# Performance work log

Hardware: AMD Instinct MI355X
Metric: run time of the kernel (lower is better)

The kernel has to match this reference:

```python
import jax, jax.numpy as jnp
import numpy as np

N = 50000
E = 800000
H = 4
C = 64
EPS = 1e-5

def _gat_layer(x, W, a_src, a_dst, bias, src, dst, n):
    # x: [N, F_in]; W: [F_in, H*C]
    h = (x @ W).reshape(n, H, C)                      # [N,H,C]
    asrc = jnp.einsum('nhc,hc->nh', h, a_src)         # [N,H]
    adst = jnp.einsum('nhc,hc->nh', h, a_dst)         # [N,H]
    e = jax.nn.leaky_relu(asrc[src] + adst[dst], 0.2) # [E,H]
    emax = jax.ops.segment_max(e, dst, num_segments=n)
    e = jnp.exp(e - emax[dst])
    denom = jax.ops.segment_sum(e, dst, num_segments=n)
    alpha = e / (denom[dst] + 1e-16)                  # [E,H]
    msg = h[src] * alpha[:, :, None]                  # [E,H,C]
    out = jax.ops.segment_sum(msg, dst, num_segments=n)
    return out.reshape(n, H * C) + bias

def _bn_eval(x, gamma, beta, mean, var):
    return (x - mean) * jax.lax.rsqrt(var + EPS) * gamma + beta

def setup_inputs() -> dict:
    key = jax.random.key(0)
    ks = jax.random.split(key, 12)
    d = {}
    d['x'] = jax.random.normal(ks[0], (N, 128), jnp.float32)
    d['edge_index'] = jax.random.randint(ks[1], (2, E), 0, N, jnp.int32)
    d['W1'] = jax.random.normal(ks[2], (128, H * C), jnp.float32) * 0.05
    d['a_src1'] = jax.random.normal(ks[3], (H, C), jnp.float32) * 0.05
    d['a_dst1'] = jax.random.normal(ks[4], (H, C), jnp.float32) * 0.05
    d['b1'] = jnp.zeros((H * C,), jnp.float32)
    d['g1'] = jax.random.uniform(ks[5], (H * C,), jnp.float32, 0.5, 1.5)
    d['be1'] = jnp.zeros((H * C,), jnp.float32)
    d['m1'] = jnp.zeros((H * C,), jnp.float32)
    d['v1'] = jax.random.uniform(ks[6], (H * C,), jnp.float32, 0.5, 1.5)
    d['W2'] = jax.random.normal(ks[7], (H * C, H * C), jnp.float32) * 0.05
    d['a_src2'] = jax.random.normal(ks[8], (H, C), jnp.float32) * 0.05
    d['a_dst2'] = jax.random.normal(ks[9], (H, C), jnp.float32) * 0.05
    d['b2'] = jnp.zeros((H * C,), jnp.float32)
    d['g2'] = jax.random.uniform(ks[10], (H * C,), jnp.float32, 0.5, 1.5)
    d['be2'] = jnp.zeros((H * C,), jnp.float32)
    d['m2'] = jnp.zeros((H * C,), jnp.float32)
    d['v2'] = jax.random.uniform(ks[11], (H * C,), jnp.float32, 0.5, 1.5)
    return d

def reference(x, edge_index, W1, a_src1, a_dst1, b1, g1, be1, m1, v1,
              W2, a_src2, a_dst2, b2, g2, be2, m2, v2):
    # PyG GATConv default: add self-loops
    loops = jnp.arange(N, dtype=edge_index.dtype)
    src = jnp.concatenate([edge_index[0], loops])
    dst = jnp.concatenate([edge_index[1], loops])
    h = _gat_layer(x, W1, a_src1, a_dst1, b1, src, dst, N)
    h = jax.nn.relu(_bn_eval(h, g1, be1, m1, v1))  # dropout identity at eval
    h = _gat_layer(h, W2, a_src2, a_dst2, b2, src, dst, N)
    h = jax.nn.relu(_bn_eval(h, g2, be2, m2, v2))
    return jax.nn.log_softmax(h, axis=1)
```

## Files before the change

kernel.cpp:

```cpp
#include <hip/hip_runtime.h>
#include <hip/hip_bf16.h>
#include <cstdint>

#define N_NODES 50000
#define N_EDGES 800000
#define ET_EDGES (N_EDGES + N_NODES)
#define FDIM 256
#define BN_EPS 1e-5f
#define CAP 96

typedef short bf16x8 __attribute__((ext_vector_type(8)));
typedef float f32x4 __attribute__((ext_vector_type(4)));

__device__ __forceinline__ float lrelu(float x) { return x >= 0.f ? x : 0.2f * x; }
__device__ __forceinline__ float b2f(unsigned short u) {
    return __uint_as_float(((unsigned int)u) << 16);
}
__device__ __forceinline__ unsigned short f2b(float f) {
    unsigned int u = __float_as_uint(f);
    u += 0x7fffu + ((u >> 16) & 1u);
    return (unsigned short)(u >> 16);
}

__device__ __forceinline__ void acc_i8(float acc8[8], int2 p, float c) {
#pragma unroll
    for (int k = 0; k < 4; ++k)
        acc8[k] = fmaf((float)((signed char)(p.x >> (8 * k))), c, acc8[k]);
#pragma unroll
    for (int k = 0; k < 4; ++k)
        acc8[k + 4] = fmaf((float)((signed char)(p.y >> (8 * k))), c, acc8[k + 4]);
}

#define NB_CONV 6250
#define NB_WT1  128
#define NB_WT2  256
#define NB_DEGZ 196
__global__ __launch_bounds__(256) void setup_kernel(
        const float* __restrict__ x, unsigned short* __restrict__ xb,
        const float* __restrict__ W1, unsigned short* __restrict__ W1T,
        const float* __restrict__ W2, unsigned short* __restrict__ W2T,
        int* __restrict__ cursor,
        const float* __restrict__ b1, const float* __restrict__ g1,
        const float* __restrict__ be1, const float* __restrict__ m1,
        const float* __restrict__ v1,
        const float* __restrict__ b2, const float* __restrict__ g2,
        const float* __restrict__ be2, const float* __restrict__ m2,
        const float* __restrict__ v2,
        float* sc1, float* sh1, float* sc2, float* sh2) {
    int b = blockIdx.x, tid = threadIdx.x;
    if (b < NB_CONV) {
        int i = b * 256 + tid;
        float4 v = ((const float4*)x)[i];
        ushort4 o;
        o.x = f2b(v.x); o.y = f2b(v.y); o.z = f2b(v.z); o.w = f2b(v.w);
        ((ushort4*)xb)[i] = o;
    } else if (b < NB_CONV + NB_WT1) {
        int t = (b - NB_CONV) * 256 + tid;
        int n = t >> 7, k = t & 127;
        W1T[t] = f2b(W1[(size_t)k * 256 + n]);
    } else if (b < NB_CONV + NB_WT1 + NB_WT2) {
        int t = (b - NB_CONV - NB_WT1) * 256 + tid;
        int n = t >> 8, k = t & 255;
        W2T[t] = f2b(W2[(size_t)k * 256 + n]);
    } else if (b < NB_CONV + NB_WT1 + NB_WT2 + NB_DEGZ) {
        int i = (b - NB_CONV - NB_WT1 - NB_WT2) * 256 + tid;
        if (i < N_NODES) cursor[i] = 0;
    } else {
        int f = tid;
        float s1 = rsqrtf(v1[f] + BN_EPS) * g1[f];
        sc1[f] = s1;
        sh1[f] = (b1[f] - m1[f]) * s1 + be1[f];
        float s2 = rsqrtf(v2[f] + BN_EPS) * g2[f];
        sc2[f] = s2;
        sh2[f] = (b2[f] - m2[f]) * s2 + be2[f];
    }
}

__global__ __launch_bounds__(256) void scatter_kernel(const int* __restrict__ ei,
                                                      int* __restrict__ cursor,
                                                      int* __restrict__ csr) {
    int e = blockIdx.x * 256 + threadIdx.x;
    if (e >= ET_EDGES) return;
    int s, d;
    if (e < N_EDGES) { s = ei[e]; d = ei[N_EDGES + e]; }
    else             { s = d = e - N_EDGES; }
    int pos = atomicAdd(&cursor[d], 1);
    if (pos < CAP) csr[d * CAP + pos] = s;
}

template <int K>
__global__ __launch_bounds__(512) void gemm_fused_kernel(
        const unsigned short* __restrict__ A,
        const unsigned short* __restrict__ BT,
        const float* __restrict__ a_src, const float* __restrict__ a_dst,
        signed char* __restrict__ H8, float* __restrict__ scaleRow,
        float* __restrict__ asrc, float* __restrict__ adst, int M) {
    constexpr int BK = 64;
    __shared__ unsigned short As[128][BK + 8];
    __shared__ unsigned short Bs[256][BK + 8];
    __shared__ int amaxL[128];
    const int tid = threadIdx.x;
    const int lane = tid & 63;
    const int w = tid >> 6;
    const int bm = blockIdx.x * 128;
    const int wr = (w >> 2) * 64;
    const int wc = (w & 3) * 64;
    const int hd = w & 3;
    if (tid < 128) amaxL[tid] = 0;

    f32x4 acc[4][4];
#pragma unroll
    for (int i = 0; i < 4; ++i)
#pragma unroll
        for (int j = 0; j < 4; ++j) acc[i][j] = (f32x4){0.f, 0.f, 0.f, 0.f};

    const int srow = tid >> 3;
    const int skc = (tid & 7) * 8;

    for (int k0 = 0; k0 < K; k0 += BK) {
#pragma unroll
        for (int i = 0; i < 2; ++i) {
            int row = i * 64 + srow;
            int ar = bm + row; if (ar >= M) ar = M - 1;
            *(bf16x8*)&As[row][skc] = *(const bf16x8*)(A + (size_t)ar * K + k0 + skc);
        }
#pragma unroll
        for (int i = 0; i < 4; ++i) {
            int row = i * 64 + srow;
            *(bf16x8*)&Bs[row][skc] = *(const bf16x8*)(BT + (size_t)row * K + k0 + skc);
        }
        __syncthreads();
#pragma unroll
        for (int ks = 0; ks < BK; ks += 32) {
            const int kk = ks + (lane >> 4) * 8;
            bf16x8 af[4], bfr[4];
#pragma unroll
            for (int i = 0; i < 4; ++i) {
                af[i]  = *(const bf16x8*)&As[wr + i * 16 + (lane & 15)][kk];
                bfr[i] = *(const bf16x8*)&Bs[wc + i * 16 + (lane & 15)][kk];
            }
#pragma unroll
            for (int i = 0; i < 4; ++i)
#pragma unroll
                for (int j = 0; j < 4; ++j)
                    acc[i][j] = __builtin_amdgcn_mfma_f32_16x16x32_bf16(af[i], bfr[j], acc[i][j], 0, 0, 0);
        }
        __syncthreads();
    }

    const int q = lane >> 4, c16 = lane & 15;
#pragma unroll
    for (int i = 0; i < 4; ++i) {
#pragma unroll
        for (int r = 0; r < 4; ++r) {
            float a = fmaxf(fmaxf(fabsf(acc[i][0][r]), fabsf(acc[i][1][r])),
                            fmaxf(fabsf(acc[i][2][r]), fabsf(acc[i][3][r])));
#pragma unroll
            for (int off = 1; off < 16; off <<= 1) a = fmaxf(a, __shfl_xor(a, off));
            if (c16 == 0) atomicMax(&amaxL[wr + i * 16 + q * 4 + r], __float_as_int(a));
        }
    }
    __syncthreads();

    float asv[4], adv[4];
#pragma unroll
    for (int j = 0; j < 4; ++j) {
        int c = j * 16 + c16;
        asv[j] = a_src[hd * 64 + c];
        adv[j] = a_dst[hd * 64 + c];
    }
#pragma unroll
    for (int i = 0; i < 4; ++i) {
#pragma unroll
        for (int r = 0; r < 4; ++r) {
            int lrow = wr + i * 16 + q * 4 + r;
            int gr = bm + lrow;
            float amax = __int_as_float(amaxL[lrow]);
            float rcpS = amax > 1e-20f ? 127.f / amax : 0.f;
            if (gr < M) {
#pragma unroll
                for (int j = 0; j < 4; ++j) {
                    int qv = (int)rintf(acc[i][j][r] * rcpS);
                    H8[(size_t)gr * 256 + wc + j * 16 + c16] = (signed char)qv;
                }
                if (c16 == 0 && (w & 3) == 0) scaleRow[gr] = amax * (1.f / 127.f);
            }
            float p_s = acc[i][0][r] * asv[0] + acc[i][1][r] * asv[1]
                      + acc[i][2][r] * asv[2] + acc[i][3][r] * asv[3];
            float p_d = acc[i][0][r] * adv[0] + acc[i][1][r] * adv[1]
                      + acc[i][2][r] * adv[2] + acc[i][3][r] * adv[3];
#pragma unroll
            for (int off = 1; off < 16; off <<= 1) {
                p_s += __shfl_xor(p_s, off);
                p_d += __shfl_xor(p_d, off);
            }
            if (c16 == 0 && gr < M) {
                asrc[(size_t)gr * 4 + hd] = p_s;
                adst[(size_t)gr * 4 + hd] = p_d;
            }
        }
    }
}

template <bool FINAL>
__device__ __forceinline__ void gat_epilogue(const float acc8[8], int fl, bool doStore,
                                             int node, const float* __restrict__ scale,
                                             const float* __restrict__ shift,
                                             float* __restrict__ outf,
                                             unsigned short* __restrict__ outb) {
    float4 scA = ((const float4*)scale)[fl * 2], scB = ((const float4*)scale)[fl * 2 + 1];
    float4 shA = ((const float4*)shift)[fl * 2], shB = ((const float4*)shift)[fl * 2 + 1];
    float t[8];
    t[0] = fmaxf(fmaf(acc8[0], scA.x, shA.x), 0.f);
    t[1] = fmaxf(fmaf(acc8[1], scA.y, shA.y), 0.f);
    t[2] = fmaxf(fmaf(acc8[2], scA.z, shA.z), 0.f);
    t[3] = fmaxf(fmaf(acc8[3], scA.w, shA.w), 0.f);
    t[4] = fmaxf(fmaf(acc8[4], scB.x, shB.x), 0.f);
    t[5] = fmaxf(fmaf(acc8[5], scB.y, shB.y), 0.f);
    t[6] = fmaxf(fmaf(acc8[6], scB.z, shB.z), 0.f);
    t[7] = fmaxf(fmaf(acc8[7], scB.w, shB.w), 0.f);
    if (FINAL) {
        float m = t[0];
#pragma unroll
        for (int k = 1; k < 8; ++k) m = fmaxf(m, t[k]);
#pragma unroll
        for (int off = 1; off < 32; off <<= 1) m = fmaxf(m, __shfl_xor(m, off));
        float es = 0.f;
#pragma unroll
        for (int k = 0; k < 8; ++k) es += __expf(t[k] - m);
#pragma unroll
        for (int off = 1; off < 32; off <<= 1) es += __shfl_xor(es, off);
        float lse = m + logf(es);
        if (doStore) {
            float* p = outf + (size_t)node * 256 + fl * 8;
            *(float4*)p = make_float4(t[0] - lse, t[1] - lse, t[2] - lse, t[3] - lse);
            *(float4*)(p + 4) = make_float4(t[4] - lse, t[5] - lse, t[6] - lse, t[7] - lse);
        }
    } else {
        if (doStore) {
            bf16x8 ob;
#pragma unroll
            for (int k = 0; k < 8; ++k) ob[k] = (short)f2b(t[k]);
            *(bf16x8*)(outb + (size_t)node * 256 + fl * 8) = ob;
        }
    }
}

template <bool FINAL>
__global__ __launch_bounds__(256) void gat_gather_kernel(const int* __restrict__ cursor,
                                                         const int* __restrict__ csr,
                                                         const float* __restrict__ asrc,
                                                         const float* __restrict__ adst,
                                                         const float* __restrict__ scaleRow,
                                                         const signed char* __restrict__ h8,
                                                         const float* __restrict__ scale,
                                                         const float* __restrict__ shift,
                                                         float* __restrict__ outf,
                                                         unsigned short* __restrict__ outb) {
    __shared__ int src_l[4][64];
    __shared__ float al[4][4][65];

    const int wid = threadIdx.x >> 6;
    const int lane = threadIdx.x & 63;
    const int nodeBase = blockIdx.x * 8 + wid * 2;
    if (nodeBase >= N_NODES) return;
    const int g = lane >> 5, l32 = lane & 31;

    {
        int node = nodeBase + g;
        bool valid = node < N_NODES;
        int nodeC = valid ? node : N_NODES - 1;
        int deg = valid ? min(cursor[nodeC], CAP) : 0;
        int beg = nodeC * CAP;
        int dmax = max(deg, __shfl_xor(deg, 32));

        if (dmax <= 32) {
            float4 ad = *(const float4*)(adst + (size_t)nodeC * 4);
            int s = 0;
            float sc = 0.f;
            float c0 = -3.4e38f, c1 = -3.4e38f, c2 = -3.4e38f, c3 = -3.4e38f;
            if (l32 < deg) {
                s = csr[beg + l32];
                sc = scaleRow[s];
                float4 as = *(const float4*)(asrc + (size_t)s * 4);
                c0 = lrelu(as.x + ad.x); c1 = lrelu(as.y + ad.y);
                c2 = lrelu(as.z + ad.z); c3 = lrelu(as.w + ad.w);
            }
            float m0 = c0, m1 = c1, m2 = c2, m3 = c3;
#pragma unroll
            for (int off = 1; off < 32; off <<= 1) {
                m0 = fmaxf(m0, __shfl_xor(m0, off)); m1 = fmaxf(m1, __shfl_xor(m1, off));
                m2 = fmaxf(m2, __shfl_xor(m2, off)); m3 = fmaxf(m3, __shfl_xor(m3, off));
            }
            float e0 = 0.f, e1 = 0.f, e2 = 0.f, e3 = 0.f;
            if (l32 < deg) {
                e0 = __expf(c0 - m0); e1 = __expf(c1 - m1);
                e2 = __expf(c2 - m2); e3 = __expf(c3 - m3);
            }
            float s0 = e0, s1 = e1, s2 = e2, s3 = e3;
#pragma unroll
            for (int off = 1; off < 32; off <<= 1) {
                s0 += __shfl_xor(s0, off); s1 += __shfl_xor(s1, off);
                s2 += __shfl_xor(s2, off); s3 += __shfl_xor(s3, off);
            }
            src_l[wid][lane] = s;
            al[wid][0][lane] = e0 / (s0 + 1e-16f) * sc;
            al[wid][1][lane] = e1 / (s1 + 1e-16f) * sc;
            al[wid][2][lane] = e2 / (s2 + 1e-16f) * sc;
            al[wid][3][lane] = e3 / (s3 + 1e-16f) * sc;
            __asm__ volatile("s_waitcnt lgkmcnt(0)" ::: "memory");

            const int base = g * 32;
            const int hsel = l32 >> 3;
            float acc8[8];
#pragma unroll
            for (int k = 0; k < 8; ++k) acc8[k] = 0.f;

            int e = 0;
            for (; e + 7 < deg; e += 8) {
                int sv[8]; float av[8]; int2 hv[8];
#pragma unroll
                for (int u = 0; u < 8; ++u) {
                    sv[u] = src_l[wid][base + e + u];
                    av[u] = al[wid][hsel][base + e + u];
                }
#pragma unroll
                for (int u = 0; u < 8; ++u)
                    hv[u] = *(const int2*)(h8 + (size_t)sv[u] * 256 + l32 * 8);
#pragma unroll
                for (int u = 0; u < 8; ++u) acc_i8(acc8, hv[u], av[u]);
            }
            for (; e + 3 < deg; e += 4) {
                int sv[4]; float av[4]; int2 hv[4];
#pragma unroll
                for (int u = 0; u < 4; ++u) {
                    sv[u] = src_l[wid][base + e + u];
                    av[u] = al[wid][hsel][base + e + u];
                }
#pragma unroll
                for (int u = 0; u < 4; ++u)
                    hv[u] = *(const int2*)(h8 + (size_t)sv[u] * 256 + l32 * 8);
#pragma unroll
                for (int u = 0; u < 4; ++u) acc_i8(acc8, hv[u], av[u]);
            }
            for (; e < deg; ++e) {
                int sA = src_l[wid][base + e];
                float aA = al[wid][hsel][base + e];
                int2 hA = *(const int2*)(h8 + (size_t)sA * 256 + l32 * 8);
                acc_i8(acc8, hA, aA);
            }
            gat_epilogue<FINAL>(acc8, l32, valid, node, scale, shift, outf, outb);
            return;
        }
    }

    const int half = lane >> 5;
    const int fl = lane & 31;
    const int hsel = fl >> 3;
    for (int t = 0; t < 2; ++t) {
        int node = nodeBase + t;
        if (node >= N_NODES) break;
        int deg = min(cursor[node], CAP);
        int beg = node * CAP, end = beg + deg;
        float4 ad = *(const float4*)(adst + (size_t)node * 4);
        float acc8[8];
#pragma unroll
        for (int k = 0; k < 8; ++k) acc8[k] = 0.f;

        if (deg <= 64) {
            int s = 0;
            float sc = 0.f;
            float c0 = -3.4e38f, c1 = -3.4e38f, c2 = -3.4e38f, c3 = -3.4e38f;
            if (lane < deg) {
                s = csr[beg + lane];
                sc = scaleRow[s];
                float4 as = *(const float4*)(asrc + (size_t)s * 4);
                c0 = lrelu(as.x + ad.x); c1 = lrelu(as.y + ad.y);
                c2 = lrelu(as.z + ad.z); c3 = lrelu(as.w + ad.w);
            }
            float m0 = c0, m1 = c1, m2 = c2, m3 = c3;
#pragma unroll
            for (int off = 1; off < 64; off <<= 1) {
                m0 = fmaxf(m0, __shfl_xor(m0, off)); m1 = fmaxf(m1, __shfl_xor(m1, off));
                m2 = fmaxf(m2, __shfl_xor(m2, off)); m3 = fmaxf(m3, __shfl_xor(m3, off));
            }
            float e0 = 0.f, e1 = 0.f, e2 = 0.f, e3 = 0.f;
            if (lane < deg) {
                e0 = __expf(c0 - m0); e1 = __expf(c1 - m1);
                e2 = __expf(c2 - m2); e3 = __expf(c3 - m3);
            }
            float s0 = e0, s1 = e1, s2 = e2, s3 = e3;
#pragma unroll
            for (int off = 1; off < 64; off <<= 1) {
                s0 += __shfl_xor(s0, off); s1 += __shfl_xor(s1, off);
                s2 += __shfl_xor(s2, off); s3 += __shfl_xor(s3, off);
            }
            src_l[wid][lane] = s;
            al[wid][0][lane] = e0 / (s0 + 1e-16f) * sc;
            al[wid][1][lane] = e1 / (s1 + 1e-16f) * sc;
            al[wid][2][lane] = e2 / (s2 + 1e-16f) * sc;
            al[wid][3][lane] = e3 / (s3 + 1e-16f) * sc;
            __asm__ volatile("s_waitcnt lgkmcnt(0)" ::: "memory");

            int e = 0;
            for (; e + 1 < deg; e += 2) {
                int iA = e + half;
                int sA = src_l[wid][iA];
                float aA = al[wid][hsel][iA];
                int2 hA = *(const int2*)(h8 + (size_t)sA * 256 + fl * 8);
                acc_i8(acc8, hA, aA);
            }
            if (e < deg) {
                int idx = e + half;
                int sA = src_l[wid][0];
                float aA = 0.f;
                if (idx < deg) { sA = src_l[wid][idx]; aA = al[wid][hsel][idx]; }
                int2 hA = *(const int2*)(h8 + (size_t)sA * 256 + fl * 8);
                acc_i8(acc8, hA, aA);
            }
#pragma unroll
            for (int k = 0; k < 8; ++k) acc8[k] += __shfl_xor(acc8[k], 32);
        } else {
            float m0 = -3.4e38f, m1 = -3.4e38f, m2 = -3.4e38f, m3 = -3.4e38f;
            for (int e = beg + lane; e < end; e += 64) {
                int s = csr[e];
                float4 as = *(const float4*)(asrc + (size_t)s * 4);
                m0 = fmaxf(m0, lrelu(as.x + ad.x)); m1 = fmaxf(m1, lrelu(as.y + ad.y));
                m2 = fmaxf(m2, lrelu(as.z + ad.z)); m3 = fmaxf(m3, lrelu(as.w + ad.w));
            }
#pragma unroll
            for (int off = 1; off < 64; off <<= 1) {
                m0 = fmaxf(m0, __shfl_xor(m0, off)); m1 = fmaxf(m1, __shfl_xor(m1, off));
                m2 = fmaxf(m2, __shfl_xor(m2, off)); m3 = fmaxf(m3, __shfl_xor(m3, off));
            }
            float s0 = 0.f, s1 = 0.f, s2 = 0.f, s3 = 0.f;
            for (int e = beg + lane; e < end; e += 64) {
                int s = csr[e];
                float4 as = *(const float4*)(asrc + (size_t)s * 4);
                s0 += __expf(lrelu(as.x + ad.x) - m0); s1 += __expf(lrelu(as.y + ad.y) - m1);
                s2 += __expf(lrelu(as.z + ad.z) - m2); s3 += __expf(lrelu(as.w + ad.w) - m3);
            }
#pragma unroll
            for (int off = 1; off < 64; off <<= 1) {
                s0 += __shfl_xor(s0, off); s1 += __shfl_xor(s1, off);
                s2 += __shfl_xor(s2, off); s3 += __shfl_xor(s3, off);
            }
            float mh = (hsel == 0) ? m0 : (hsel == 1) ? m1 : (hsel == 2) ? m2 : m3;
            float rh = (hsel == 0) ? 1.f / (s0 + 1e-16f) : (hsel == 1) ? 1.f / (s1 + 1e-16f)
                     : (hsel == 2) ? 1.f / (s2 + 1e-16f) : 1.f / (s3 + 1e-16f);
            float adh = (hsel == 0) ? ad.x : (hsel == 1) ? ad.y : (hsel == 2) ? ad.z : ad.w;
            for (int e = beg; e < end; ++e) {
                int s = csr[e];
                float ash = asrc[(size_t)s * 4 + hsel];
                float a = __expf(lrelu(ash + adh) - mh) * rh * scaleRow[s];
                int2 hv = *(const int2*)(h8 + (size_t)s * 256 + fl * 8);
                acc_i8(acc8, hv, a);
            }
        }
        gat_epilogue<FINAL>(acc8, fl, half == 0, node, scale, shift, outf, outb);
    }
}

extern "C" void kernel_launch(void* const* d_in, const int* in_sizes, int n_in,
                              void* d_out, int out_size, void* d_ws, size_t ws_size,
                              hipStream_t stream) {
    (void)in_sizes; (void)n_in; (void)out_size; (void)ws_size;
    const float* x   = (const float*)d_in[0];
    const int*   ei  = (const int*)d_in[1];
    const float* W1  = (const float*)d_in[2];
    const float* as1 = (const float*)d_in[3];
    const float* ad1 = (const float*)d_in[4];
    const float* b1  = (const float*)d_in[5];
    const float* g1  = (const float*)d_in[6];
    const float* be1 = (const float*)d_in[7];
    const float* m1  = (const float*)d_in[8];
    const float* v1  = (const float*)d_in[9];
    const float* W2  = (const float*)d_in[10];
    const float* as2 = (const float*)d_in[11];
    const float* ad2 = (const float*)d_in[12];
    const float* b2  = (const float*)d_in[13];
    const float* g2  = (const float*)d_in[14];
    const float* be2 = (const float*)d_in[15];
    const float* m2  = (const float*)d_in[16];
    const float* v2  = (const float*)d_in[17];

    float* out = (float*)d_out;
    unsigned short* actb = (unsigned short*)d_out;

    char* base = (char*)d_ws;
    signed char* h8 = (signed char*)base;          base += (size_t)N_NODES * 256;
    float* scaleRow = (float*)base;                base += (size_t)N_NODES * 4;
    unsigned short* xb  = (unsigned short*)base;   base += (size_t)N_NODES * 128 * 2;
    float* asrc = (float*)base;                    base += (size_t)N_NODES * 4 * 4;
    float* adst = (float*)base;                    base += (size_t)N_NODES * 4 * 4;
    float* sc1 = (float*)base;                     base += 1024;
    float* sh1 = (float*)base;                     base += 1024;
    float* sc2 = (float*)base;                     base += 1024;
    float* sh2 = (float*)base;                     base += 1024;
    unsigned short* W1T = (unsigned short*)base;   base += 256 * 128 * 2;
    unsigned short* W2T = (unsigned short*)base;   base += 256 * 256 * 2;
    int* cursor = (int*)base;                      base += N_NODES * 4;
    int* csr  = (int*)base;

    setup_kernel<<<NB_CONV + NB_WT1 + NB_WT2 + NB_DEGZ + 1, 256, 0, stream>>>(
        x, xb, W1, W1T, W2, W2T, cursor,
        b1, g1, be1, m1, v1, b2, g2, be2, m2, v2, sc1, sh1, sc2, sh2);

    const int eb = (ET_EDGES + 255) / 256;
    scatter_kernel<<<eb, 256, 0, stream>>>(ei, cursor, csr);

    const int gb = (N_NODES + 127) / 128;
    const int nb = (N_NODES + 7) / 8;

    gemm_fused_kernel<128><<<gb, 512, 0, stream>>>(xb, W1T, as1, ad1, h8, scaleRow,
                                                   asrc, adst, N_NODES);
    gat_gather_kernel<false><<<nb, 256, 0, stream>>>(cursor, csr, asrc, adst, scaleRow, h8,
                                                     sc1, sh1, nullptr, actb);

    gemm_fused_kernel<256><<<gb, 512, 0, stream>>>(actb, W2T, as2, ad2, h8, scaleRow,
                                                   asrc, adst, N_NODES);
    gat_gather_kernel<true><<<nb, 256, 0, stream>>>(cursor, csr, asrc, adst, scaleRow, h8,
                                                    sc2, sh2, out, nullptr);
}
```

Before: 323.3 us.

## Use offset-uint8 features, packed LDS src/alpha, persistent grid in GAT gather

Quantized features are now stored with a +128 offset so the gather can decode them as unsigned bytes, which is cheaper than sign-extending them. The offset is removed afterwards by subtracting 128 times the sum of the alphas. The source index and alpha are packed together into one int2 LDS entry, and address math uses 32-bit shifts. The gather kernel becomes a grid-stride loop with a fixed 2048 blocks and launch bounds of 8 waves. Risks are the extra alpha reduction and rounding error from the correction term.

```diff
diff --git a/kernel.cpp b/kernel.cpp
--- a/kernel.cpp
+++ b/kernel.cpp
@@ -22,13 +22,14 @@
     return (unsigned short)(u >> 16);
 }
 
-__device__ __forceinline__ void acc_i8(float acc8[8], int2 p, float c) {
+__device__ __forceinline__ void acc_u8(float acc8[8], int2 p, float c) {
+    unsigned px = (unsigned)p.x, py = (unsigned)p.y;
 #pragma unroll
     for (int k = 0; k < 4; ++k)
-        acc8[k] = fmaf((float)((signed char)(p.x >> (8 * k))), c, acc8[k]);
+        acc8[k] = fmaf((float)((unsigned char)(px >> (8 * k))), c, acc8[k]);
 #pragma unroll
     for (int k = 0; k < 4; ++k)
-        acc8[k + 4] = fmaf((float)((signed char)(p.y >> (8 * k))), c, acc8[k + 4]);
+        acc8[k + 4] = fmaf((float)((unsigned char)(py >> (8 * k))), c, acc8[k + 4]);
 }
 
 #define NB_CONV 6250
@@ -181,7 +182,8 @@
 #pragma unroll
                 for (int j = 0; j < 4; ++j) {
                     int qv = (int)rintf(acc[i][j][r] * rcpS);
-                    H8[(size_t)gr * 256 + wc + j * 16 + c16] = (signed char)qv;
+                    H8[(size_t)gr * 256 + wc + j * 16 + c16] =
+                        (signed char)(unsigned char)(qv + 128);
                 }
                 if (c16 == 0 && (w & 3) == 0) scaleRow[gr] = amax * (1.f / 127.f);
             }
@@ -247,26 +249,29 @@
 }
 
 template <bool FINAL>
-__global__ __launch_bounds__(256) void gat_gather_kernel(const int* __restrict__ cursor,
-                                                         const int* __restrict__ csr,
-                                                         const float* __restrict__ asrc,
-                                                         const float* __restrict__ adst,
-                                                         const float* __restrict__ scaleRow,
-                                                         const signed char* __restrict__ h8,
-                                                         const float* __restrict__ scale,
-                                                         const float* __restrict__ shift,
-                                                         float* __restrict__ outf,
-                                                         unsigned short* __restrict__ outb) {
-    __shared__ int src_l[4][64];
-    __shared__ float al[4][4][65];
+__global__ __launch_bounds__(256, 8) void gat_gather_kernel(
+        const int* __restrict__ cursor,
+        const int* __restrict__ csr,
+        const float* __restrict__ asrc,
+        const float* __restrict__ adst,
+        const float* __restrict__ scaleRow,
+        const signed char* __restrict__ h8,
+        const float* __restrict__ scale,
+        const float* __restrict__ shift,
+        float* __restrict__ outf,
+        unsigned short* __restrict__ outb) {
+    __shared__ int2 sa[4][4][65];
 
     const int wid = threadIdx.x >> 6;
     const int lane = threadIdx.x & 63;
-    const int nodeBase = blockIdx.x * 8 + wid * 2;
-    if (nodeBase >= N_NODES) return;
     const int g = lane >> 5, l32 = lane & 31;
-
-    {
+    const int hsel = l32 >> 3;
+    const unsigned fo = (unsigned)(l32 << 3);
+
+    for (int nb0 = blockIdx.x * 8; nb0 < N_NODES; nb0 += gridDim.x * 8) {
+        const int nodeBase = nb0 + wid * 2;
+        if (nodeBase >= N_NODES) continue;
+
         int node = nodeBase + g;
         bool valid = node < N_NODES;
         int nodeC = valid ? node : N_NODES - 1;
@@ -303,161 +308,172 @@
                 s0 += __shfl_xor(s0, off); s1 += __shfl_xor(s1, off);
                 s2 += __shfl_xor(s2, off); s3 += __shfl_xor(s3, off);
             }
-            src_l[wid][lane] = s;
-            al[wid][0][lane] = e0 / (s0 + 1e-16f) * sc;
-            al[wid][1][lane] = e1 / (s1 + 1e-16f) * sc;
-            al[wid][2][lane] = e2 / (s2 + 1e-16f) * sc;
-            al[wid][3][lane] = e3 / (s3 + 1e-16f) * sc;
+            float a0 = e0 / (s0 + 1e-16f) * sc, a1 = e1 / (s1 + 1e-16f) * sc;
+            float a2 = e2 / (s2 + 1e-16f) * sc, a3 = e3 / (s3 + 1e-16f) * sc;
+            sa[wid][0][lane] = make_int2(s, __float_as_int(a0));
+            sa[wid][1][lane] = make_int2(s, __float_as_int(a1));
+            sa[wid][2][lane] = make_int2(s, __float_as_int(a2));
+            sa[wid][3][lane] = make_int2(s, __float_as_int(a3));
+            float t0 = a0, t1 = a1, t2 = a2, t3 = a3;
+#pragma unroll
+            for (int off = 1; off < 32; off <<= 1) {
+                t0 += __shfl_xor(t0, off); t1 += __shfl_xor(t1, off);
+                t2 += __shfl_xor(t2, off); t3 += __shfl_xor(t3, off);
+            }
+            float corr = 128.f * (hsel == 0 ? t0 : hsel == 1 ? t1 : hsel == 2 ? t2 : t3);
             __asm__ volatile("s_waitcnt lgkmcnt(0)" ::: "memory");
 
-            const int base = g * 32;
-            const int hsel = l32 >> 3;
+            const int2* sal = &sa[wid][hsel][g * 32];
             float acc8[8];
 #pragma unroll
             for (int k = 0; k < 8; ++k) acc8[k] = 0.f;
 
             int e = 0;
             for (; e + 7 < deg; e += 8) {
-                int sv[8]; float av[8]; int2 hv[8];
-#pragma unroll
-                for (int u = 0; u < 8; ++u) {
-                    sv[u] = src_l[wid][base + e + u];
-                    av[u] = al[wid][hsel][base + e + u];
-                }
+                int2 sv[8]; int2 hv[8];
+#pragma unroll
+                for (int u = 0; u < 8; ++u) sv[u] = sal[e + u];
 #pragma unroll
                 for (int u = 0; u < 8; ++u)
-                    hv[u] = *(const int2*)(h8 + (size_t)sv[u] * 256 + l32 * 8);
-#pragma unroll
-                for (int u = 0; u < 8; ++u) acc_i8(acc8, hv[u], av[u]);
+                    hv[u] = *(const int2*)(h8 + (((unsigned)sv[u].x << 8) + fo));
+#pragma unroll
+                for (int u = 0; u < 8; ++u) acc_u8(acc8, hv[u], __int_as_float(sv[u].y));
             }
             for (; e + 3 < deg; e += 4) {
-                int sv[4]; float av[4]; int2 hv[4];
-#pragma unroll
-                for (int u = 0; u < 4; ++u) {
-                    sv[u] = src_l[wid][base + e + u];
-                    av[u] = al[wid][hsel][base + e + u];
-                }
+                int2 sv[4]; int2 hv[4];
+#pragma unroll
+                for (int u = 0; u < 4; ++u) sv[u] = sal[e + u];
 #pragma unroll
                 for (int u = 0; u < 4; ++u)
-                    hv[u] = *(const int2*)(h8 + (size_t)sv[u] * 256 + l32 * 8);
-#pragma unroll
-                for (int u = 0; u < 4; ++u) acc_i8(acc8, hv[u], av[u]);
+                    hv[u] = *(const int2*)(h8 + (((unsigned)sv[u].x << 8) + fo));
+#pragma unroll
+                for (int u = 0; u < 4; ++u) acc_u8(acc8, hv[u], __int_as_float(sv[u].y));
             }
             for (; e < deg; ++e) {
-                int sA = src_l[wid][base + e];
-                float aA = al[wid][hsel][base + e];
-                int2 hA = *(const int2*)(h8 + (size_t)sA * 256 + l32 * 8);
-                acc_i8(acc8, hA, aA);
-            }
+                int2 sv = sal[e];
+                int2 hA = *(const int2*)(h8 + (((unsigned)sv.x << 8) + fo));
+                acc_u8(acc8, hA, __int_as_float(sv.y));
+            }
+#pragma unroll
+            for (int k = 0; k < 8; ++k) acc8[k] -= corr;
             gat_epilogue<FINAL>(acc8, l32, valid, node, scale, shift, outf, outb);
-            return;
-        }
-    }
-
-    const int half = lane >> 5;
-    const int fl = lane & 31;
-    const int hsel = fl >> 3;
-    for (int t = 0; t < 2; ++t) {
-        int node = nodeBase + t;
-        if (node >= N_NODES) break;
-        int deg = min(cursor[node], CAP);
-        int beg = node * CAP, end = beg + deg;
-        float4 ad = *(const float4*)(adst + (size_t)node * 4);
-        float acc8[8];
-#pragma unroll
-        for (int k = 0; k < 8; ++k) acc8[k] = 0.f;
-
-        if (deg <= 64) {
-            int s = 0;
-            float sc = 0.f;
-            float c0 = -3.4e38f, c1 = -3.4e38f, c2 = -3.4e38f, c3 = -3.4e38f;
-            if (lane < deg) {
-                s = csr[beg + lane];
-                sc = scaleRow[s];
-                float4 as = *(const float4*)(asrc + (size_t)s * 4);
-                c0 = lrelu(as.x + ad.x); c1 = lrelu(as.y + ad.y);
-                c2 = lrelu(as.z + ad.z); c3 = lrelu(as.w + ad.w);
-            }
-            float m0 = c0, m1 = c1, m2 = c2, m3 = c3;
-#pragma unroll
-            for (int off = 1; off < 64; off <<= 1) {
-                m0 = fmaxf(m0, __shfl_xor(m0, off)); m1 = fmaxf(m1, __shfl_xor(m1, off));
-                m2 = fmaxf(m2, __shfl_xor(m2, off)); m3 = fmaxf(m3, __shfl_xor(m3, off));
-            }
-            float e0 = 0.f, e1 = 0.f, e2 = 0.f, e3 = 0.f;
-            if (lane < deg) {
-                e0 = __expf(c0 - m0); e1 = __expf(c1 - m1);
-                e2 = __expf(c2 - m2); e3 = __expf(c3 - m3);
-            }
-            float s0 = e0, s1 = e1, s2 = e2, s3 = e3;
-#pragma unroll
-            for (int off = 1; off < 64; off <<= 1) {
-                s0 += __shfl_xor(s0, off); s1 += __shfl_xor(s1, off);
-                s2 += __shfl_xor(s2, off); s3 += __shfl_xor(s3, off);
-            }
-            src_l[wid][lane] = s;
-            al[wid][0][lane] = e0 / (s0 + 1e-16f) * sc;
-            al[wid][1][lane] = e1 / (s1 + 1e-16f) * sc;
-            al[wid][2][lane] = e2 / (s2 + 1e-16f) * sc;
-            al[wid][3][lane] = e3 / (s3 + 1e-16f) * sc;
-            __asm__ volatile("s_waitcnt lgkmcnt(0)" ::: "memory");
-
-            int e = 0;
-            for (; e + 1 < deg; e += 2) {
-                int iA = e + half;
-                int sA = src_l[wid][iA];
-                float aA = al[wid][hsel][iA];
-                int2 hA = *(const int2*)(h8 + (size_t)sA * 256 + fl * 8);
-                acc_i8(acc8, hA, aA);
-            }
-            if (e < deg) {
-                int idx = e + half;
-                int sA = src_l[wid][0];
-                float aA = 0.f;
-                if (idx < deg) { sA = src_l[wid][idx]; aA = al[wid][hsel][idx]; }
-                int2 hA = *(const int2*)(h8 + (size_t)sA * 256 + fl * 8);
-                acc_i8(acc8, hA, aA);
-            }
-#pragma unroll
-            for (int k = 0; k < 8; ++k) acc8[k] += __shfl_xor(acc8[k], 32);
-        } else {
-            float m0 = -3.4e38f, m1 = -3.4e38f, m2 = -3.4e38f, m3 = -3.4e38f;
-            for (int e = beg + lane; e < end; e += 64) {
-                int s = csr[e];
-                float4 as = *(const float4*)(asrc + (size_t)s * 4);
-                m0 = fmaxf(m0, lrelu(as.x + ad.x)); m1 = fmaxf(m1, lrelu(as.y + ad.y));
-                m2 = fmaxf(m2, lrelu(as.z + ad.z)); m3 = fmaxf(m3, lrelu(as.w + ad.w));
-            }
-#pragma unroll
-            for (int off = 1; off < 64; off <<= 1) {
-                m0 = fmaxf(m0, __shfl_xor(m0, off)); m1 = fmaxf(m1, __shfl_xor(m1, off));
-                m2 = fmaxf(m2, __shfl_xor(m2, off)); m3 = fmaxf(m3, __shfl_xor(m3, off));
-            }
-            float s0 = 0.f, s1 = 0.f, s2 = 0.f, s3 = 0.f;
-            for (int e = beg + lane; e < end; e += 64) {
-                int s = csr[e];
-                float4 as = *(const float4*)(asrc + (size_t)s * 4);
-                s0 += __expf(lrelu(as.x + ad.x) - m0); s1 += __expf(lrelu(as.y + ad.y) - m1);
-                s2 += __expf(lrelu(as.z + ad.z) - m2); s3 += __expf(lrelu(as.w + ad.w) - m3);
-            }
-#pragma unroll
-            for (int off = 1; off < 64; off <<= 1) {
-                s0 += __shfl_xor(s0, off); s1 += __shfl_xor(s1, off);
-                s2 += __shfl_xor(s2, off); s3 += __shfl_xor(s3, off);
-            }
-            float mh = (hsel == 0) ? m0 : (hsel == 1) ? m1 : (hsel == 2) ? m2 : m3;
-            float rh = (hsel == 0) ? 1.f / (s0 + 1e-16f) : (hsel == 1) ? 1.f / (s1 + 1e-16f)
-                     : (hsel == 2) ? 1.f / (s2 + 1e-16f) : 1.f / (s3 + 1e-16f);
-            float adh = (hsel == 0) ? ad.x : (hsel == 1) ? ad.y : (hsel == 2) ? ad.z : ad.w;
-            for (int e = beg; e < end; ++e) {
-                int s = csr[e];
-                float ash = asrc[(size_t)s * 4 + hsel];
-                float a = __expf(lrelu(ash + adh) - mh) * rh * scaleRow[s];
-                int2 hv = *(const int2*)(h8 + (size_t)s * 256 + fl * 8);
-                acc_i8(acc8, hv, a);
-            }
-        }
-        gat_epilogue<FINAL>(acc8, fl, half == 0, node, scale, shift, outf, outb);
+            continue;
+        }
+
+        for (int t = 0; t < 2; ++t) {
+            int fnode = nodeBase + t;
+            if (fnode >= N_NODES) break;
+            int fdeg = min(cursor[fnode], CAP);
+            int fbeg = fnode * CAP, fend = fbeg + fdeg;
+            float4 ad = *(const float4*)(adst + (size_t)fnode * 4);
+            float acc8[8];
+#pragma unroll
+            for (int k = 0; k < 8; ++k) acc8[k] = 0.f;
+            float corr;
+
+            if (fdeg <= 64) {
+                int s = 0;
+                float sc = 0.f;
+                float c0 = -3.4e38f, c1 = -3.4e38f, c2 = -3.4e38f, c3 = -3.4e38f;
+                if (lane < fdeg) {
+                    s = csr[fbeg + lane];
+                    sc = scaleRow[s];
+                    float4 as = *(const float4*)(asrc + (size_t)s * 4);
+                    c0 = lrelu(as.x + ad.x); c1 = lrelu(as.y + ad.y);
+                    c2 = lrelu(as.z + ad.z); c3 = lrelu(as.w + ad.w);
+                }
+                float m0 = c0, m1 = c1, m2 = c2, m3 = c3;
+#pragma unroll
+                for (int off = 1; off < 64; off <<= 1) {
+                    m0 = fmaxf(m0, __shfl_xor(m0, off)); m1 = fmaxf(m1, __shfl_xor(m1, off));
+                    m2 = fmaxf(m2, __shfl_xor(m2, off)); m3 = fmaxf(m3, __shfl_xor(m3, off));
+                }
+                float e0 = 0.f, e1 = 0.f, e2 = 0.f, e3 = 0.f;
+                if (lane < fdeg) {
+                    e0 = __expf(c0 - m0); e1 = __expf(c1 - m1);
+                    e2 = __expf(c2 - m2); e3 = __expf(c3 - m3);
+                }
+                float s0 = e0, s1 = e1, s2 = e2, s3 = e3;
+#pragma unroll
+                for (int off = 1; off < 64; off <<= 1) {
+                    s0 += __shfl_xor(s0, off); s1 += __shfl_xor(s1, off);
+                    s2 += __shfl_xor(s2, off); s3 += __shfl_xor(s3, off);
+                }
+                float a0 = e0 / (s0 + 1e-16f) * sc, a1 = e1 / (s1 + 1e-16f) * sc;
+                float a2 = e2 / (s2 + 1e-16f) * sc, a3 = e3 / (s3 + 1e-16f) * sc;
+                sa[wid][0][lane] = make_int2(s, __float_as_int(a0));
+                sa[wid][1][lane] = make_int2(s, __float_as_int(a1));
+                sa[wid][2][lane] = make_int2(s, __float_as_int(a2));
+                sa[wid][3][lane] = make_int2(s, __float_as_int(a3));
+                float t0 = a0, t1 = a1, t2 = a2, t3 = a3;
+#pragma unroll
+                for (int off = 1; off < 64; off <<= 1) {
+                    t0 += __shfl_xor(t0, off); t1 += __shfl_xor(t1, off);
+                    t2 += __shfl_xor(t2, off); t3 += __shfl_xor(t3, off);
+                }
+                corr = 128.f * (hsel == 0 ? t0 : hsel == 1 ? t1 : hsel == 2 ? t2 : t3);
+                __asm__ volatile("s_waitcnt lgkmcnt(0)" ::: "memory");
+
+                const int2* sal = &sa[wid][hsel][0];
+                int e = 0;
+                for (; e + 1 < fdeg; e += 2) {
+                    int2 sv = sal[e + g];
+                    int2 hA = *(const int2*)(h8 + (((unsigned)sv.x << 8) + fo));
+                    acc_u8(acc8, hA, __int_as_float(sv.y));
+                }
+                if (e < fdeg) {
+                    int idx = e + g;
+                    int2 sv = sal[idx < fdeg ? idx : 0];
+                    float aA = idx < fdeg ? __int_as_float(sv.y) : 0.f;
+                    int2 hA = *(const int2*)(h8 + (((unsigned)sv.x << 8) + fo));
+                    acc_u8(acc8, hA, aA);
+                }
+#pragma unroll
+                for (int k = 0; k < 8; ++k) acc8[k] += __shfl_xor(acc8[k], 32);
+            } else {
+                float m0 = -3.4e38f, m1 = -3.4e38f, m2 = -3.4e38f, m3 = -3.4e38f;
+                for (int e = fbeg + lane; e < fend; e += 64) {
+                    int s = csr[e];
+                    float4 as = *(const float4*)(asrc + (size_t)s * 4);
+                    m0 = fmaxf(m0, lrelu(as.x + ad.x)); m1 = fmaxf(m1, lrelu(as.y + ad.y));
+                    m2 = fmaxf(m2, lrelu(as.z + ad.z)); m3 = fmaxf(m3, lrelu(as.w + ad.w));
+                }
+#pragma unroll
+                for (int off = 1; off < 64; off <<= 1) {
+                    m0 = fmaxf(m0, __shfl_xor(m0, off)); m1 = fmaxf(m1, __shfl_xor(m1, off));
+                    m2 = fmaxf(m2, __shfl_xor(m2, off)); m3 = fmaxf(m3, __shfl_xor(m3, off));
+                }
+                float s0 = 0.f, s1 = 0.f, s2 = 0.f, s3 = 0.f;
+                for (int e = fbeg + lane; e < fend; e += 64) {
+                    int s = csr[e];
+                    float4 as = *(const float4*)(asrc + (size_t)s * 4);
+                    s0 += __expf(lrelu(as.x + ad.x) - m0); s1 += __expf(lrelu(as.y + ad.y) - m1);
+                    s2 += __expf(lrelu(as.z + ad.z) - m2); s3 += __expf(lrelu(as.w + ad.w) - m3);
+                }
+#pragma unroll
+                for (int off = 1; off < 64; off <<= 1) {
+                    s0 += __shfl_xor(s0, off); s1 += __shfl_xor(s1, off);
+                    s2 += __shfl_xor(s2, off); s3 += __shfl_xor(s3, off);
+                }
+                float mh = (hsel == 0) ? m0 : (hsel == 1) ? m1 : (hsel == 2) ? m2 : m3;
+                float rh = (hsel == 0) ? 1.f / (s0 + 1e-16f) : (hsel == 1) ? 1.f / (s1 + 1e-16f)
+                         : (hsel == 2) ? 1.f / (s2 + 1e-16f) : 1.f / (s3 + 1e-16f);
+                float adh = (hsel == 0) ? ad.x : (hsel == 1) ? ad.y : (hsel == 2) ? ad.z : ad.w;
+                float asumL = 0.f;
+                for (int e = fbeg; e < fend; ++e) {
+                    int s = csr[e];
+                    float ash = asrc[(size_t)s * 4 + hsel];
+                    float a = __expf(lrelu(ash + adh) - mh) * rh * scaleRow[s];
+                    asumL += a;
+                    int2 hv = *(const int2*)(h8 + (((unsigned)s << 8) + fo));
+                    acc_u8(acc8, hv, a);
+                }
+                corr = 128.f * asumL;
+            }
+#pragma unroll
+            for (int k = 0; k < 8; ++k) acc8[k] -= corr;
+            gat_epilogue<FINAL>(acc8, l32, g == 0, fnode, scale, shift, outf, outb);
+        }
     }
 }
 
@@ -510,7 +526,7 @@
     scatter_kernel<<<eb, 256, 0, stream>>>(ei, cursor, csr);
 
     const int gb = (N_NODES + 127) / 128;
-    const int nb = (N_NODES + 7) / 8;
+    const int nb = 2048;
 
     gemm_fused_kernel<128><<<gb, 512, 0, stream>>>(xb, W1T, as1, ad1, h8, scaleRow,
                                                    asrc, adst, N_NODES);
```

Result: slower. 351.0 us (+8.5%).
